# Performance work log

Hardware: AMD Instinct MI355X
Metric: run time of the kernel (lower is better)

Reference implementation:

```python
import jax, jax.numpy as jnp
import numpy as np

B, CIN, COUT, H, W = 16, 128, 128, 64, 64
E, PS, FF = 8, 16, 8
GC, HID, HC = 4 * FF, 64, COUT * 4  # gate_channel, gate hidden, bottleneck hidden


def conv(x, w, stride=1, pad=0, groups=1):
    # x: [B,C,H,W], w: [O,I/groups,kh,kw]
    return jax.lax.conv_general_dilated(
        x, w, (stride, stride), [(pad, pad), (pad, pad)], feature_group_count=groups)


def group_norm(x, scale, bias, groups, eps=1e-5):
    b, c = x.shape[:2]
    xr = x.reshape(b, groups, c // groups, *x.shape[2:])
    m = xr.mean(axis=(2, 3, 4), keepdims=True)
    v = xr.var(axis=(2, 3, 4), keepdims=True)
    xr = (xr - m) * jax.lax.rsqrt(v + eps)
    return xr.reshape(x.shape) * scale[None, :, None, None] + bias[None, :, None, None]


def setup_inputs() -> dict:
    key = jax.random.key(0)
    ks = jax.random.split(key, 8)
    f = lambda k, shp: jax.random.normal(k, shp, jnp.float32) * 0.05
    return dict(
        x=jax.random.normal(ks[0], (B, CIN, H, W), jnp.float32),
        w_exp=f(ks[1], (E, COUT, CIN, 3, 3)),
        gn_exp_s=jnp.ones((E, COUT), jnp.float32),
        gn_exp_b=jnp.zeros((E, COUT), jnp.float32),
        w1=f(ks[2], (GC, HID)), b1=jnp.zeros((HID,), jnp.float32),
        w2=f(ks[3], (HID, E)), b2=jnp.zeros((E,), jnp.float32),
        w_pw1=f(ks[4], (HC, COUT, 1, 1)),
        gn1_s=jnp.ones((HC,), jnp.float32), gn1_b=jnp.zeros((HC,), jnp.float32),
        w_dw=f(ks[5], (HC, 1, 3, 3)),
        gn2_s=jnp.ones((HC,), jnp.float32), gn2_b=jnp.zeros((HC,), jnp.float32),
        w_pw2=f(ks[6], (COUT, HC, 1, 1)),
        gn3_s=jnp.ones((COUT,), jnp.float32), gn3_b=jnp.zeros((COUT,), jnp.float32),
    )


def reference(x, w_exp, gn_exp_s, gn_exp_b, w1, b1, w2, b2,
              w_pw1, gn1_s, gn1_b, w_dw, gn2_s, gn2_b, w_pw2, gn3_s, gn3_b):
    # ---- Conv experts (residual 3x3 conv + GN + SiLU), vmapped over experts ----
    def expert(w, s, b):
        y = conv(x, w, pad=1)
        y = group_norm(y, s, b, groups=min(8, COUT))
        return jax.nn.silu(y) + x  # use_residual=True, CIN == COUT

    ys = jax.vmap(expert)(w_exp, gn_exp_s, gn_exp_b)  # [E,B,C,H,W]

    # ---- Router gate: Fourier features of patch-center coordinates ----
    ph, pw = H // PS, W // PS
    cy = (jnp.arange(ph, dtype=jnp.float32) + 0.5) / ph
    cx = (jnp.arange(pw, dtype=jnp.float32) + 0.5) / pw
    freqs = (2.0 ** jnp.arange(FF, dtype=jnp.float32)) * jnp.pi
    ay = cy[:, None] * freqs  # [ph,FF]
    ax = cx[:, None] * freqs  # [pw,FF]
    feats = jnp.concatenate([
        jnp.broadcast_to(jnp.sin(ay)[:, None, :], (ph, pw, FF)),
        jnp.broadcast_to(jnp.cos(ay)[:, None, :], (ph, pw, FF)),
        jnp.broadcast_to(jnp.sin(ax)[None, :, :], (ph, pw, FF)),
        jnp.broadcast_to(jnp.cos(ax)[None, :, :], (ph, pw, FF)),
    ], axis=-1)  # [ph,pw,4*FF] == gate_channel
    hgate = jax.nn.silu(feats @ w1 + b1)
    wts = jax.nn.softmax(hgate @ w2 + b2, axis=-1)  # [ph,pw,E]

    # ---- Patch-wise combine of expert outputs ----
    wmap = jnp.repeat(jnp.repeat(wts, PS, axis=0), PS, axis=1)  # [H,W,E]
    combined = jnp.einsum('ebchw,hwe->bchw', ys, wmap)

    # ---- Inverted bottleneck: 1x1 -> dw3x3 -> 1x1(stride2) with GN+SiLU ----
    h = jax.nn.silu(group_norm(conv(combined, w_pw1), gn1_s, gn1_b, groups=8))
    h = jax.nn.silu(group_norm(conv(h, w_dw, pad=1, groups=HC), gn2_s, gn2_b, groups=8))
    h = jax.nn.silu(group_norm(conv(h, w_pw2, stride=2), gn3_s, gn3_b, groups=8))
    return h  # [B, COUT, H//2, W//2]
```

## Files before the change

### kernel.cpp

```cpp
#include <hip/hip_runtime.h>
#include <hip/hip_bf16.h>


#define B_ 16
#define CIN_ 128
#define COUT_ 128
#define H_ 64
#define W_ 64
#define HW_ 4096
#define E_ 8
#define FF_ 8
#define GC_ 32
#define HID_ 64
#define HC_ 512

typedef __hip_bfloat16 bf16;
typedef __bf16 bf16x8 __attribute__((ext_vector_type(8)));
typedef float f32x4 __attribute__((ext_vector_type(4)));
typedef float f32x16 __attribute__((ext_vector_type(16)));

__device__ __forceinline__ float siluf(float v) {
  return v * __builtin_amdgcn_rcpf(1.f + __expf(-v));
}
__device__ __forceinline__ float bf2f(bf16 v) { return __bfloat162float(v); }
__device__ __forceinline__ bf16 f2bf(float v) { return __float2bfloat16(v); }

__device__ __forceinline__ void async16(void* lds, const void* g) {
  __builtin_amdgcn_global_load_lds(
      (const __attribute__((address_space(1))) unsigned int*)g,
      (__attribute__((address_space(3))) unsigned int*)lds, 16, 0, 0);
}

__global__ __launch_bounds__(256) void prep_kernel(
    const float* __restrict__ x, bf16* __restrict__ xT,
    const float* __restrict__ w_exp, bf16* __restrict__ wT,
    const float* __restrict__ w_pw1, const float* __restrict__ w_pw2,
    bf16* __restrict__ wp1T, bf16* __restrict__ wp2T,
    const float* __restrict__ w1, const float* __restrict__ b1,
    const float* __restrict__ w2, const float* __restrict__ b2,
    float* __restrict__ wts) {
  __shared__ float t[128][65];
  int blk = blockIdx.x;
  int tid = threadIdx.x;

  if (blk < 1024) {
    int b = blk >> 6, h = blk & 63;
    int w = tid & 63, c4 = tid >> 6;
    const float* xb = x + ((size_t)(b * 128) * 64 + h) * 64;
#pragma unroll 4
    for (int rep = 0; rep < 32; ++rep) {
      int ci = rep * 4 + c4;
      t[ci][w] = xb[(size_t)ci * HW_ + w];
    }
    __syncthreads();
    bf16* dst = xT + (size_t)(b * 64 + h) * 8192;
#pragma unroll 4
    for (int rep = 0; rep < 32; ++rep) {
      int o = rep * 256 + tid;
      int cg = o >> 9, w2 = (o >> 3) & 63, lo = o & 7;
      dst[o] = f2bf(t[cg * 8 + lo][w2]);
    }
  } else if (blk < 5632) {
    int idx = (blk - 1024) * 256 + tid;
    if (idx < 1179648) {
      int lo = idx & 7;
      int co = (idx >> 3) & 127;
      int cg = (idx >> 10) & 15;
      int rest = idx >> 14;
      int tap = rest % 9, e = rest / 9;
      int ci = cg * 8 + lo;
      wT[idx] = f2bf(w_exp[(((size_t)(e * 128 + co) * 128 + ci) * 9) + tap]);
    }
  } else if (blk < 6144) {
    int idx = (blk - 5632) * 256 + tid;
    if (idx < 65536) wp1T[idx] = f2bf(w_pw1[idx]);
    else wp2T[idx - 65536] = f2bf(w_pw2[idx - 65536]);
  } else {
    uint4* z = (uint4*)((char*)wts + 1024);
    for (int i = tid; i < 960; i += 256) z[i] = make_uint4(0u, 0u, 0u, 0u);
    int p = tid;
    if (p >= 16) return;
    int i = p >> 2, j = p & 3;
    float cy = (i + 0.5f) * 0.25f;
    float cx = (j + 0.5f) * 0.25f;
    float feats[GC_];
#pragma unroll
    for (int f = 0; f < FF_; ++f) {
      float fr = 3.14159265358979f * (float)(1 << f);
      float ay = cy * fr, ax = cx * fr;
      feats[f] = sinf(ay);
      feats[FF_ + f] = cosf(ay);
      feats[2 * FF_ + f] = sinf(ax);
      feats[3 * FF_ + f] = cosf(ax);
    }
    float hid[HID_];
    for (int k = 0; k < HID_; ++k) {
      float a = b1[k];
#pragma unroll
      for (int m = 0; m < GC_; ++m) a = fmaf(feats[m], w1[m * HID_ + k], a);
      hid[k] = siluf(a);
    }
    float lg[E_];
    float mx = -1e30f;
#pragma unroll
    for (int e = 0; e < E_; ++e) {
      float a = b2[e];
      for (int k = 0; k < HID_; ++k) a = fmaf(hid[k], w2[k * E_ + e], a);
      lg[e] = a;
      mx = fmaxf(mx, a);
    }
    float s = 0.f;
#pragma unroll
    for (int e = 0; e < E_; ++e) { lg[e] = __expf(lg[e] - mx); s += lg[e]; }
    float inv = 1.f / s;
#pragma unroll
    for (int e = 0; e < E_; ++e) wts[p * E_ + e] = lg[e] * inv;
  }
}

__global__ __launch_bounds__(256, 2) void conv_mfma(
    const bf16* __restrict__ xT, const bf16* __restrict__ wT,
    float* __restrict__ statsE, bf16* __restrict__ ys, int e_base) {
  __shared__ __align__(16) char xls[4 * 6336];
  __shared__ __align__(16) char wls[2][3 * 8192];
  __shared__ float red[4][8][2];

  int blk = blockIdx.x;
  int xcd = blk & 7;
  int r2 = blk >> 3;
  int b = xcd * 2 + (r2 & 1);
  int rest = r2 >> 1;
  int rt = rest & 15, e = e_base + (rest >> 4);

  int tid = threadIdx.x, lane = tid & 63, wave = tid >> 6;
  int hi = lane >> 5, l31 = lane & 31;
  int h0 = rt * 4;

  if (tid < 48) {
    int cg = tid / 12, rem = tid % 12;
    int r = rem >> 1, edge = rem & 1;
    *(uint4*)(xls + cg * 6336 + r * 1056 + edge * 1040) = make_uint4(0u, 0u, 0u, 0u);
  }
  int rbad = (rt == 0) ? 0 : (rt == 15 ? 5 : -1);
  if (rbad >= 0) {
    int cg = tid >> 6, slot = (tid & 63) + 1;
    *(uint4*)(xls + cg * 6336 + rbad * 1056 + slot * 16) = make_uint4(0u, 0u, 0u, 0u);
  }

  f32x16 acc[4][2];
#pragma unroll
  for (int mt = 0; mt < 4; ++mt)
#pragma unroll
    for (int nt = 0; nt < 2; ++nt)
#pragma unroll
      for (int r = 0; r < 16; ++r) acc[mt][nt][r] = 0.f;

  for (int q = 0; q < 4; ++q) {
    if (q) __syncthreads();
    {
      int cg = wave;
#pragma unroll
      for (int r = 0; r < 6; ++r) {
        int h = h0 - 1 + r;
        if ((unsigned)h < 64u) {
          const char* g = (const char*)xT +
              ((size_t)((b * 64 + h) * 16) + q * 4 + cg) * 1024 + lane * 16;
          async16(xls + cg * 6336 + r * 1056 + 16, g);
        }
      }
    }
#pragma unroll
    for (int s = 0; s < 6; ++s) {
      int seg = wave * 6 + s;
      int tap = seg >> 3, rem = seg & 7;
      int cg = rem >> 1, cb = rem & 1;
      const char* g = (const char*)wT +
          ((size_t)(((e * 9 + tap) * 16) + q * 4 + cg) * 128 + cb * 64) * 16 + lane * 16;
      async16(wls[0] + (tap * 4 + cg) * 2048 + cb * 1024, g);
    }
    __syncthreads();

    for (int dr = 0; dr < 3; ++dr) {
      int buf = dr & 1;
      if (dr < 2) {
#pragma unroll
        for (int s = 0; s < 6; ++s) {
          int seg = wave * 6 + s;
          int tap = seg >> 3, rem = seg & 7;
          int cg = rem >> 1, cb = rem & 1;
          const char* g = (const char*)wT +
              ((size_t)(((e * 9 + (dr + 1) * 3 + tap) * 16) + q * 4 + cg) * 128 + cb * 64) * 16 +
              lane * 16;
          async16(wls[buf ^ 1] + (tap * 4 + cg) * 2048 + cb * 1024, g);
        }
      }
      int r_local = wave + dr;
      const char* wb = wls[buf];
      const char* xrow = xls;
      bf16x8 afp[2][2], bfp[2][2];
      {
        int cgl = hi;
        afp[0][0] = *(const bf16x8*)(wb + cgl * 2048 + (0 * 32 + l31) * 16);
        afp[0][1] = *(const bf16x8*)(wb + cgl * 2048 + (1 * 32 + l31) * 16);
        const char* xr = xrow + cgl * 6336 + r_local * 1056;
        bfp[0][0] = *(const bf16x8*)(xr + (0 * 32 + l31 + 0) * 16);
        bfp[0][1] = *(const bf16x8*)(xr + (1 * 32 + l31 + 0) * 16);
      }
#pragma unroll
      for (int s = 0; s < 12; ++s) {
        int mh = s & 1;
        int cura = s & 1, curb = (s >> 1) & 1;
        if (s < 11) {
          int s1 = s + 1;
          int ds1 = s1 >> 2, ks1 = (s1 >> 1) & 1, mh1 = s1 & 1;
          int cgl1 = ks1 * 2 + hi;
          const char* wt1 = wb + ds1 * 8192 + cgl1 * 2048;
          afp[s1 & 1][0] = *(const bf16x8*)(wt1 + ((mh1 * 2 + 0) * 32 + l31) * 16);
          afp[s1 & 1][1] = *(const bf16x8*)(wt1 + ((mh1 * 2 + 1) * 32 + l31) * 16);
          if (mh1 == 0) {
            const char* xr1 = xrow + cgl1 * 6336 + r_local * 1056;
            bfp[(s1 >> 1) & 1][0] = *(const bf16x8*)(xr1 + (0 * 32 + l31 + ds1) * 16);
            bfp[(s1 >> 1) & 1][1] = *(const bf16x8*)(xr1 + (1 * 32 + l31 + ds1) * 16);
          }
        }
#pragma unroll
        for (int i = 0; i < 2; ++i)
#pragma unroll
          for (int nt = 0; nt < 2; ++nt)
            acc[mh * 2 + i][nt] = __builtin_amdgcn_mfma_f32_32x32x16_bf16(
                afp[cura][i], bfp[curb][nt], acc[mh * 2 + i][nt], 0, 0, 0);
      }
      if (dr < 2) __syncthreads();
    }
  }

  int hh = h0 + wave;
  bf16* yb = ys + (size_t)((e * 16 + b) * 128) * 4096;
#pragma unroll
  for (int mt = 0; mt < 4; ++mt) {
    float s0 = 0.f, ss0 = 0.f, s1 = 0.f, ss1 = 0.f;
#pragma unroll
    for (int nt = 0; nt < 2; ++nt) {
      int w = nt * 32 + l31;
      int pos = hh * 64 + w;
#pragma unroll
      for (int r = 0; r < 16; ++r) {
        float v = acc[mt][nt][r];
        if (r < 8) { s0 += v; ss0 += v * v; } else { s1 += v; ss1 += v * v; }
        int row = (r & 3) + 8 * (r >> 2) + 4 * hi;
        yb[(size_t)(mt * 32 + row) * 4096 + pos] = f2bf(v);
      }
    }
#pragma unroll
    for (int off = 32; off; off >>= 1) {
      s0 += __shfl_down(s0, off, 64);
      ss0 += __shfl_down(ss0, off, 64);
      s1 += __shfl_down(s1, off, 64);
      ss1 += __shfl_down(ss1, off, 64);
    }
    if (lane == 0) {
      red[wave][mt * 2][0] = s0; red[wave][mt * 2][1] = ss0;
      red[wave][mt * 2 + 1][0] = s1; red[wave][mt * 2 + 1][1] = ss1;
    }
  }
  __syncthreads();
  if (tid < 16) {
    int g = tid >> 1, which = tid & 1;
    float t = red[0][g][which] + red[1][g][which] + red[2][g][which] + red[3][g][which];
    atomicAdd(&statsE[((e * 16 + b) * 8 + g) * 2 + which], t);
  }
}

__global__ __launch_bounds__(256) void combine_cl(
    const float* __restrict__ x, const bf16* __restrict__ ys,
    const float* __restrict__ stE, const float* __restrict__ gns,
    const float* __restrict__ gnb, const float* __restrict__ wts,
    bf16* __restrict__ ccl) {
  __shared__ bf16 tile[64][132];
  int blk = blockIdx.x;
  int xcd = blk & 7;
  int k2 = blk >> 3;
  int b = xcd * 2 + (k2 >> 6);
  int h = k2 & 63;
  int t = threadIdx.x;
  int oct = t & 7, cq = t >> 3;
  int w0 = oct * 8;
  int gidx = cq >> 2;
  int pid = (h >> 4) * 4 + (w0 >> 4);
  int pos = h * 64 + w0;

  float m_[8], r_[8], wt_[8];
#pragma unroll
  for (int e = 0; e < 8; ++e) {
    float S = stE[((e * 16 + b) * 8 + gidx) * 2];
    float SS = stE[((e * 16 + b) * 8 + gidx) * 2 + 1];
    float mean = S * (1.f / 65536.f);
    float var = SS * (1.f / 65536.f) - mean * mean;
    m_[e] = mean;
    r_[e] = rsqrtf(var + 1e-5f);
    wt_[e] = wts[pid * 8 + e];
  }

#pragma unroll
  for (int k = 0; k < 4; ++k) {
    int co = cq * 4 + k;
    const float* xp = x + ((size_t)(b * 128 + co) << 12) + pos;
    float v[8];
    float4 xa = *(const float4*)xp;
    float4 xb2 = *(const float4*)(xp + 4);
    v[0] = xa.x; v[1] = xa.y; v[2] = xa.z; v[3] = xa.w;
    v[4] = xb2.x; v[5] = xb2.y; v[6] = xb2.z; v[7] = xb2.w;
#pragma unroll
    for (int e = 0; e < 8; ++e) {
      uint4 u = *(const uint4*)(ys + ((size_t)((e * 16 + b) * 128 + co) << 12) + pos);
      const bf16* pv = (const bf16*)&u;
      float sc = r_[e] * gns[e * 128 + co];
      float sh = gnb[e * 128 + co] - m_[e] * sc;
#pragma unroll
      for (int j = 0; j < 8; ++j) {
        float yn = bf2f(pv[j]) * sc + sh;
        v[j] = fmaf(siluf(yn), wt_[e], v[j]);
      }
    }
#pragma unroll
    for (int j = 0; j < 8; ++j) tile[w0 + j][co] = f2bf(v[j]);
  }
  __syncthreads();
  int row = t >> 2, q = t & 3;
  char* dst = (char*)ccl + ((size_t)(b * 4096 + h * 64 + row)) * 256 + q * 64;
  const char* src = (const char*)&tile[row][0] + q * 64;
#pragma unroll
  for (int i = 0; i < 4; ++i)
    *(uint4*)(dst + i * 16) = *(const uint4*)(src + i * 16);
}

__global__ __launch_bounds__(256) void pw1_mfma(
    const bf16* __restrict__ ccl, const bf16* __restrict__ wp1T,
    bf16* __restrict__ h1cl, float* __restrict__ stats1) {
  __shared__ __align__(16) char bls[32768];
  __shared__ __align__(16) char ls2[34816];
  __shared__ float red[4][2][2];
  int blk = blockIdx.x;
  int n0 = blk * 128;
  int t = threadIdx.x, lane = t & 63, wave = t >> 6;
  int quad = lane >> 4, l15 = lane & 15;
  int b = n0 >> 12;

#pragma unroll
  for (int i = 0; i < 8; ++i) {
    int id = t + 256 * i;
    int r = id >> 4, c = id & 15;
    *(uint4*)(bls + c * 2048 + r * 16) =
        *(const uint4*)((const char*)ccl + (size_t)(n0 + r) * 256 + c * 16);
  }

  for (int mtile = 0; mtile < 4; ++mtile) {
    int m0 = mtile * 128;
    char* als = ls2;
#pragma unroll
    for (int i = 0; i < 8; ++i) {
      int id = t + 256 * i;
      int r = id >> 4, c = id & 15;
      *(uint4*)(als + c * 2048 + r * 16) =
          *(const uint4*)((const char*)wp1T + (size_t)(m0 + r) * 256 + c * 16);
    }
    __syncthreads();

    f32x4 acc[8][2];
#pragma unroll
    for (int mt = 0; mt < 8; ++mt)
#pragma unroll
      for (int nt = 0; nt < 2; ++nt) acc[mt][nt] = (f32x4){0.f, 0.f, 0.f, 0.f};

#pragma unroll
    for (int kc = 0; kc < 4; ++kc) {
      int cgq = kc * 4 + quad;
      bf16x8 af[8];
#pragma unroll
      for (int mt = 0; mt < 8; ++mt)
        af[mt] = *(const bf16x8*)(als + cgq * 2048 + (mt * 16 + l15) * 16);
      bf16x8 bfr[2];
#pragma unroll
      for (int nt = 0; nt < 2; ++nt)
        bfr[nt] = *(const bf16x8*)(bls + cgq * 2048 + (wave * 32 + nt * 16 + l15) * 16);
#pragma unroll
      for (int mt = 0; mt < 8; ++mt)
#pragma unroll
        for (int nt = 0; nt < 2; ++nt)
          acc[mt][nt] = __builtin_amdgcn_mfma_f32_16x16x32_bf16(
              af[mt], bfr[nt], acc[mt][nt], 0, 0, 0);
    }

    __syncthreads();
    float s[2] = {0.f, 0.f}, ss[2] = {0.f, 0.f};
    bf16* tile = (bf16*)ls2;
#pragma unroll
    for (int mt = 0; mt < 8; ++mt) {
      int gi = mt >> 2;
#pragma unroll
      for (int nt = 0; nt < 2; ++nt) {
        int n = wave * 32 + nt * 16 + l15;
#pragma unroll
        for (int r = 0; r < 4; ++r) {
          float v = acc[mt][nt][r];
          s[gi] += v;
          ss[gi] += v * v;
          tile[n * 132 + mt * 16 + quad * 4 + r] = f2bf(v);
        }
      }
    }
#pragma unroll
    for (int gi = 0; gi < 2; ++gi) {
#pragma unroll
      for (int off = 32; off; off >>= 1) {
        s[gi] += __shfl_down(s[gi], off, 64);
        ss[gi] += __shfl_down(ss[gi], off, 64);
      }
    }
    if (lane == 0) {
      red[wave][0][0] = s[0]; red[wave][0][1] = ss[0];
      red[wave][1][0] = s[1]; red[wave][1][1] = ss[1];
    }
    __syncthreads();
    if (t < 4) {
      int gi = t >> 1, which = t & 1;
      float v = red[0][gi][which] + red[1][gi][which] + red[2][gi][which] + red[3][gi][which];
      atomicAdd(&stats1[(b * 8 + mtile * 2 + gi) * 2 + which], v);
    }
#pragma unroll
    for (int i = 0; i < 8; ++i) {
      int id = t + 256 * i;
      int r = id >> 4, q = id & 15;
      char* dst = (char*)h1cl + (size_t)(n0 + r) * 1024 + m0 * 2 + q * 16;
      const char* src = (const char*)tile + r * 264 + q * 16;
      *(uint4*)dst = *(const uint4*)src;
    }
    __syncthreads();
  }
}

__global__ __launch_bounds__(256) void dw_cl(
    const bf16* __restrict__ h1cl, const float* __restrict__ w_dw,
    const float* __restrict__ st1, const float* __restrict__ gs,
    const float* __restrict__ gb, bf16* __restrict__ h2cl,
    float* __restrict__ stats2) {
  __shared__ __align__(16) bf16 tile[18 * 66 * 16];
  __shared__ float red2[4][2];
  int blk = blockIdx.x;
  int ht = blk & 3, hcg = (blk >> 2) & 31, b = blk >> 7;
  int h0 = ht * 16;
  int hc0 = hcg * 16;
  int hcb = hcg >> 2;
  int t = threadIdx.x;

  float S1 = st1[(b * 8 + hcb) * 2], SS1 = st1[(b * 8 + hcb) * 2 + 1];
  float mean = S1 * (1.f / 262144.f);
  float var1 = SS1 * (1.f / 262144.f) - mean * mean;
  float rstd = rsqrtf(var1 + 1e-5f);
  float scale[16], shift[16];
#pragma unroll
  for (int j = 0; j < 16; ++j) {
    float g = gs[hc0 + j];
    scale[j] = rstd * g;
    shift[j] = gb[hc0 + j] - mean * rstd * g;
  }

  for (int i = 0; i < 5; ++i) {
    int idx = t + 256 * i;
    if (idx >= 1188) break;
    int row = idx / 66, wslot = idx - row * 66;
    int hh = h0 - 1 + row;
    int w = wslot - 1;
    int swz = (wslot >> 2) & 3;
    bf16* dst = tile + (row * 66 + wslot) * 16;
    if ((unsigned)hh < 64u && (unsigned)w < 64u) {
      const char* p = (const char*)h1cl + ((size_t)(b * 4096 + hh * 64 + w) * 512 + hc0) * 2;
      uint4 a0 = *(const uint4*)p;
      uint4 a1 = *(const uint4*)(p + 16);
      const bf16* pv = (const bf16*)&a0;
      const bf16* pv1 = (const bf16*)&a1;
      bf16 outv[16];
#pragma unroll
      for (int j = 0; j < 8; ++j)
        outv[j] = f2bf(siluf(bf2f(pv[j]) * scale[j] + shift[j]));
#pragma unroll
      for (int j = 0; j < 8; ++j)
        outv[8 + j] = f2bf(siluf(bf2f(pv1[j]) * scale[8 + j] + shift[8 + j]));
#pragma unroll
      for (int qq = 0; qq < 4; ++qq) {
        int ph = (qq + swz) & 3;
        *(uint2*)(dst + ph * 4) = *(const uint2*)(outv + qq * 4);
      }
    } else {
      *(uint4*)dst = make_uint4(0u, 0u, 0u, 0u);
      *(uint4*)(dst + 8) = make_uint4(0u, 0u, 0u, 0u);
    }
  }
  __syncthreads();

  int w = t & 63, q = t >> 6;
  float wv[9][4];
#pragma unroll
  for (int j = 0; j < 4; ++j) {
    int hc = hc0 + q * 4 + j;
#pragma unroll
    for (int tap = 0; tap < 9; ++tap) wv[tap][j] = w_dw[hc * 9 + tap];
  }

  f32x4 win[3][3];
  float acc_s = 0.f, acc_ss = 0.f;

  auto ld4 = [&](int r, int dwi) -> f32x4 {
    int slot = w + dwi;
    int ph = (q + (slot >> 2)) & 3;
    const bf16* p = tile + (r * 66 + slot) * 16 + ph * 4;
    uint2 u = *(const uint2*)p;
    const bf16* pb = (const bf16*)&u;
    return (f32x4){bf2f(pb[0]), bf2f(pb[1]), bf2f(pb[2]), bf2f(pb[3])};
  };

#pragma unroll
  for (int dwi = 0; dwi < 3; ++dwi) {
    win[0][dwi] = ld4(0, dwi);
    win[1][dwi] = ld4(1, dwi);
  }
#pragma unroll
  for (int orow = 0; orow < 16; ++orow) {
    int rnew = orow + 2;
    int ringn = rnew % 3;
#pragma unroll
    for (int dwi = 0; dwi < 3; ++dwi) win[ringn][dwi] = ld4(rnew, dwi);
    f32x4 acc = (f32x4){0.f, 0.f, 0.f, 0.f};
#pragma unroll
    for (int dr = 0; dr < 3; ++dr) {
      int ring = (orow + dr) % 3;
#pragma unroll
      for (int dwi = 0; dwi < 3; ++dwi) {
#pragma unroll
        for (int j = 0; j < 4; ++j)
          acc[j] = fmaf(win[ring][dwi][j], wv[dr * 3 + dwi][j], acc[j]);
      }
    }
#pragma unroll
    for (int j = 0; j < 4; ++j) { acc_s += acc[j]; acc_ss += acc[j] * acc[j]; }
    if (!(orow & 1) && !(w & 1)) {
      int hglob = h0 + orow;
      int pos2 = (hglob >> 1) * 32 + (w >> 1);
      bf16 tmp[4];
#pragma unroll
      for (int j = 0; j < 4; ++j) tmp[j] = f2bf(acc[j]);
      *(uint2*)((char*)h2cl + ((size_t)(b * 1024 + pos2) * 512 + hc0 + q * 4) * 2) =
          *(const uint2*)tmp;
    }
  }

#pragma unroll
  for (int off = 32; off; off >>= 1) {
    acc_s += __shfl_down(acc_s, off, 64);
    acc_ss += __shfl_down(acc_ss, off, 64);
  }
  int wave = t >> 6;
  if ((t & 63) == 0) { red2[wave][0] = acc_s; red2[wave][1] = acc_ss; }
  __syncthreads();
  if (t < 2) {
    float v = red2[0][t] + red2[1][t] + red2[2][t] + red2[3][t];
    atomicAdd(&stats2[(b * 8 + hcb) * 2 + t], v);
  }
}

__global__ __launch_bounds__(256) void pw2_mfma(
    const bf16* __restrict__ h2, const bf16* __restrict__ wp2T,
    const float* __restrict__ st2, const float* __restrict__ gs2,
    const float* __restrict__ gb2, float* __restrict__ h3,
    float* __restrict__ stats3) {
  __shared__ __align__(16) char als[2][4096];
  __shared__ __align__(16) char bls[2][4096];
  __shared__ float red[4][4][2];
  int blk = blockIdx.x;
  int mhalf = blk >> 8;
  int nblk = blk & 255;
  int n0 = nblk * 64;
  int m0 = mhalf * 64;
  int b = n0 >> 10, posb = n0 & 1023;
  int t = threadIdx.x, lane = t & 63, wave = t >> 6;
  int quad = lane >> 4, l15 = lane & 15;
  int wbase = wave * 16;
  int c4 = t >> 6, r = t & 63;

  auto load_bls = [&](char* dst, int kc) {
    int hc0 = (kc * 4 + c4) * 8;
    int g = hc0 >> 6;
    float S = st2[(b * 8 + g) * 2], SS = st2[(b * 8 + g) * 2 + 1];
    float mean = S * (1.f / 262144.f);
    float rstd = rsqrtf(SS * (1.f / 262144.f) - mean * mean + 1e-5f);
    uint4 u = *(const uint4*)((const char*)h2 + (size_t)(n0 + r) * 1024 +
                              (size_t)(kc * 4 + c4) * 16);
    const bf16* pv = (const bf16*)&u;
    bf16 outv[8];
#pragma unroll
    for (int j = 0; j < 8; ++j) {
      float xv = bf2f(pv[j]);
      xv = (xv - mean) * rstd * gs2[hc0 + j] + gb2[hc0 + j];
      outv[j] = f2bf(siluf(xv));
    }
    *(uint4*)dst = *(const uint4*)outv;
  };
  auto load_als = [&](char* dstbase, int kc) {
    *(uint4*)(dstbase + c4 * 1024 + r * 16) =
        *(const uint4*)((const char*)wp2T + (size_t)(m0 + r) * 1024 +
                        (size_t)(kc * 4 + c4) * 16);
  };

  f32x4 acc[4];
#pragma unroll
  for (int mt = 0; mt < 4; ++mt) acc[mt] = (f32x4){0.f, 0.f, 0.f, 0.f};

  {
    load_als(als[0], 0);
    load_bls(bls[0] + c4 * 1024 + r * 16, 0);
  }
#pragma unroll
  for (int kc = 0; kc < 16; ++kc) {
    __syncthreads();
    if (kc + 1 < 16) {
      int nb = (kc + 1) & 1;
      load_als(als[nb], kc + 1);
      load_bls(bls[nb] + c4 * 1024 + r * 16, kc + 1);
    }
    int buf = kc & 1;
    bf16x8 bf1 = *(const bf16x8*)(bls[buf] + quad * 1024 + (wbase + l15) * 16);
#pragma unroll
    for (int mt = 0; mt < 4; ++mt) {
      bf16x8 af = *(const bf16x8*)(als[buf] + quad * 1024 + (mt * 16 + l15) * 16);
      acc[mt] = __builtin_amdgcn_mfma_f32_16x16x32_bf16(af, bf1, acc[mt], 0, 0, 0);
    }
  }

#pragma unroll
  for (int mt = 0; mt < 4; ++mt) {
    float s = 0.f, ss = 0.f;
    int pos = posb + wbase + l15;
#pragma unroll
    for (int rr = 0; rr < 4; ++rr) {
      float v = acc[mt][rr];
      s += v;
      ss += v * v;
      int co = m0 + mt * 16 + quad * 4 + rr;
      h3[(size_t)(b * 128 + co) * 1024 + pos] = v;
    }
#pragma unroll
    for (int off = 32; off; off >>= 1) {
      s += __shfl_down(s, off, 64);
      ss += __shfl_down(ss, off, 64);
    }
    if (lane == 0) { red[wave][mt][0] = s; red[wave][mt][1] = ss; }
  }
  __syncthreads();
  if (t < 8) {
    int mt = t >> 1, which = t & 1;
    float v = red[0][mt][which] + red[1][mt][which] + red[2][mt][which] + red[3][mt][which];
    atomicAdd(&stats3[(b * 8 + mhalf * 4 + mt) * 2 + which], v);
  }
}

__global__ void out_kernel(const float* __restrict__ h3, const float* __restrict__ stats,
                           const float* __restrict__ gs, const float* __restrict__ gb,
                           float* __restrict__ out) {
  const int total4 = (B_ * COUT_ * 1024) >> 2;
  for (int i4 = blockIdx.x * blockDim.x + threadIdx.x; i4 < total4;
       i4 += gridDim.x * blockDim.x) {
    int idx = i4 << 2;
    int c = (idx >> 10) & 127;
    int b = idx >> 17;
    int bg = b * 8 + (c >> 4);
    float S = stats[bg * 2], SS = stats[bg * 2 + 1];
    float mean = S * (1.f / 16384.f);
    float var = SS * (1.f / 16384.f) - mean * mean;
    float rstd = rsqrtf(var + 1e-5f);
    float sc = rstd * gs[c];
    float sh = gb[c] - mean * sc;
    float4 hv = *(const float4*)(h3 + idx);
    float4 res;
    res.x = siluf(hv.x * sc + sh);
    res.y = siluf(hv.y * sc + sh);
    res.z = siluf(hv.z * sc + sh);
    res.w = siluf(hv.w * sc + sh);
    *(float4*)(out + idx) = res;
  }
}

extern "C" void kernel_launch(void* const* d_in, const int* in_sizes, int n_in,
                              void* d_out, int out_size, void* d_ws, size_t ws_size,
                              hipStream_t stream) {
  const float* x = (const float*)d_in[0];
  const float* w_exp = (const float*)d_in[1];
  const float* gn_exp_s = (const float*)d_in[2];
  const float* gn_exp_b = (const float*)d_in[3];
  const float* w1 = (const float*)d_in[4];
  const float* b1 = (const float*)d_in[5];
  const float* w2 = (const float*)d_in[6];
  const float* b2 = (const float*)d_in[7];
  const float* w_pw1 = (const float*)d_in[8];
  const float* gn1_s = (const float*)d_in[9];
  const float* gn1_b = (const float*)d_in[10];
  const float* w_dw = (const float*)d_in[11];
  const float* gn2_s = (const float*)d_in[12];
  const float* gn2_b = (const float*)d_in[13];
  const float* w_pw2 = (const float*)d_in[14];
  const float* gn3_s = (const float*)d_in[15];
  const float* gn3_b = (const float*)d_in[16];

  char* ws = (char*)d_ws;
  const size_t WP1T_OFF = 16384;
  const size_t WP2T_OFF = WP1T_OFF + 131072;
  const size_t XT_OFF = WP2T_OFF + 131072;
  const size_t WT_OFF = XT_OFF + 16777216;
  const size_t YS_OFF = WT_OFF + 2359296;
  const size_t NEEDED = YS_OFF + 134217728;
  if (ws_size < NEEDED) return;

  float* wts = (float*)ws;
  float* stats1 = (float*)(ws + 1024);
  float* stats2 = (float*)(ws + 2048);
  float* stats3 = (float*)(ws + 3072);
  float* statsE = (float*)(ws + 4096);
  bf16* wp1T = (bf16*)(ws + WP1T_OFF);
  bf16* wp2T = (bf16*)(ws + WP2T_OFF);
  bf16* xT = (bf16*)(ws + XT_OFF);
  bf16* ccl = (bf16*)(ws + XT_OFF);
  bf16* wT = (bf16*)(ws + WT_OFF);
  bf16* ys = (bf16*)(ws + YS_OFF);
  bf16* h1cl = (bf16*)(ws + YS_OFF);
  bf16* h2cl = (bf16*)(ws + YS_OFF + 67108864);
  float* h3 = (float*)(ws + YS_OFF + 83886080);

  prep_kernel<<<6145, 256, 0, stream>>>(x, xT, w_exp, wT, w_pw1, w_pw2, wp1T, wp2T,
                                        w1, b1, w2, b2, wts);
  conv_mfma<<<1024, 256, 0, stream>>>(xT, wT, statsE, ys, 0);
  conv_mfma<<<1024, 256, 0, stream>>>(xT, wT, statsE, ys, 4);
  combine_cl<<<B_ * 64, 256, 0, stream>>>(x, ys, statsE, gn_exp_s, gn_exp_b, wts, ccl);
  pw1_mfma<<<512, 256, 0, stream>>>(ccl, wp1T, h1cl, stats1);
  dw_cl<<<B_ * 32 * 4, 256, 0, stream>>>(h1cl, w_dw, stats1, gn1_s, gn1_b, h2cl, stats2);
  pw2_mfma<<<512, 256, 0, stream>>>(h2cl, wp2T, stats2, gn2_s, gn2_b, h3, stats3);
  out_kernel<<<1024, 256, 0, stream>>>(h3, stats3, gn3_s, gn3_b, (float*)d_out);
}
```

Baseline: 432.9 us.

## Fuse expert combine into pw1 GEMM and merge expert conv launches

Adds a combine_pw1 kernel that builds the GN+SiLU+gated expert combination for two image rows directly in shared memory and immediately runs the 1x1 pw1 MFMA GEMM on it. This avoids writing the combined tensor to global memory and reading it back. The two conv_mfma launches are also merged into one 2048-block grid. The fused path needs a larger workspace so h1 does not overwrite ys, and it falls back to the old path if the workspace is too small.

Measured after the change: 451.3 us. +4.3%, slower.

```diff
diff --git a/kernel.cpp b/kernel.cpp
--- a/kernel.cpp
+++ b/kernel.cpp
@@ -120,7 +120,7 @@
 
 __global__ __launch_bounds__(256, 2) void conv_mfma(
     const bf16* __restrict__ xT, const bf16* __restrict__ wT,
-    float* __restrict__ statsE, bf16* __restrict__ ys, int e_base) {
+    float* __restrict__ statsE, bf16* __restrict__ ys) {
   __shared__ __align__(16) char xls[4 * 6336];
   __shared__ __align__(16) char wls[2][3 * 8192];
   __shared__ float red[4][8][2];
@@ -130,7 +130,7 @@
   int r2 = blk >> 3;
   int b = xcd * 2 + (r2 & 1);
   int rest = r2 >> 1;
-  int rt = rest & 15, e = e_base + (rest >> 4);
+  int rt = rest & 15, e = rest >> 4;
 
   int tid = threadIdx.x, lane = tid & 63, wave = tid >> 6;
   int hi = lane >> 5, l31 = lane & 31;
@@ -268,6 +268,161 @@
     int g = tid >> 1, which = tid & 1;
     float t = red[0][g][which] + red[1][g][which] + red[2][g][which] + red[3][g][which];
     atomicAdd(&statsE[((e * 16 + b) * 8 + g) * 2 + which], t);
+  }
+}
+
+__global__ __launch_bounds__(256) void combine_pw1(
+    const float* __restrict__ x, const bf16* __restrict__ ys,
+    const float* __restrict__ stE, const float* __restrict__ gns,
+    const float* __restrict__ gnb, const float* __restrict__ wts,
+    const bf16* __restrict__ wp1T, bf16* __restrict__ h1cl,
+    float* __restrict__ stats1) {
+  __shared__ __align__(16) char bls[32768];
+  __shared__ __align__(16) char ls2[34816];
+  __shared__ float red[4][2][2];
+
+  int blk = blockIdx.x;
+  int xcd = blk & 7;
+  int rest = blk >> 3;
+  int b = xcd * 2 + (rest & 1);
+  int hpair = rest >> 1;
+  int h0 = hpair * 2;
+  int n0 = b * 4096 + h0 * 64;
+
+  int t = threadIdx.x, lane = t & 63, wave = t >> 6;
+  int quad = lane >> 4, l15 = lane & 15;
+
+  {
+    int oct = t & 7, cq = t >> 3;
+    int w0 = oct * 8;
+    int gidx = cq >> 2;
+    int pid = (h0 >> 4) * 4 + (w0 >> 4);
+
+    float m_[8], r_[8], wt_[8];
+#pragma unroll
+    for (int e = 0; e < 8; ++e) {
+      float S = stE[((e * 16 + b) * 8 + gidx) * 2];
+      float SS = stE[((e * 16 + b) * 8 + gidx) * 2 + 1];
+      float mean = S * (1.f / 65536.f);
+      float var = SS * (1.f / 65536.f) - mean * mean;
+      m_[e] = mean;
+      r_[e] = rsqrtf(var + 1e-5f);
+      wt_[e] = wts[pid * 8 + e];
+    }
+
+#pragma unroll
+    for (int hh = 0; hh < 2; ++hh) {
+      int pos = (h0 + hh) * 64 + w0;
+#pragma unroll
+      for (int k = 0; k < 4; ++k) {
+        int co = cq * 4 + k;
+        const float* xp = x + ((size_t)(b * 128 + co) << 12) + pos;
+        float v[8];
+        float4 xa = *(const float4*)xp;
+        float4 xb2 = *(const float4*)(xp + 4);
+        v[0] = xa.x; v[1] = xa.y; v[2] = xa.z; v[3] = xa.w;
+        v[4] = xb2.x; v[5] = xb2.y; v[6] = xb2.z; v[7] = xb2.w;
+#pragma unroll
+        for (int e = 0; e < 8; ++e) {
+          uint4 u = *(const uint4*)(ys + ((size_t)((e * 16 + b) * 128 + co) << 12) + pos);
+          const bf16* pv = (const bf16*)&u;
+          float sc = r_[e] * gns[e * 128 + co];
+          float sh = gnb[e * 128 + co] - m_[e] * sc;
+#pragma unroll
+          for (int j = 0; j < 8; ++j) {
+            float yn = bf2f(pv[j]) * sc + sh;
+            v[j] = fmaf(siluf(yn), wt_[e], v[j]);
+          }
+        }
+        bf16* bb = (bf16*)bls + (co >> 3) * 1024 + (hh * 64 + w0) * 8 + (co & 7);
+#pragma unroll
+        for (int j = 0; j < 8; ++j) bb[j * 8] = f2bf(v[j]);
+      }
+    }
+  }
+
+  for (int mtile = 0; mtile < 4; ++mtile) {
+    int m0 = mtile * 128;
+    char* als = ls2;
+#pragma unroll
+    for (int i = 0; i < 8; ++i) {
+      int id = t + 256 * i;
+      int r = id >> 4, c = id & 15;
+      *(uint4*)(als + c * 2048 + r * 16) =
+          *(const uint4*)((const char*)wp1T + (size_t)(m0 + r) * 256 + c * 16);
+    }
+    __syncthreads();
+
+    f32x4 acc[8][2];
+#pragma unroll
+    for (int mt = 0; mt < 8; ++mt)
+#pragma unroll
+      for (int nt = 0; nt < 2; ++nt) acc[mt][nt] = (f32x4){0.f, 0.f, 0.f, 0.f};
+
+#pragma unroll
+    for (int kc = 0; kc < 4; ++kc) {
+      int cgq = kc * 4 + quad;
+      bf16x8 af[8];
+#pragma unroll
+      for (int mt = 0; mt < 8; ++mt)
+        af[mt] = *(const bf16x8*)(als + cgq * 2048 + (mt * 16 + l15) * 16);
+      bf16x8 bfr[2];
+#pragma unroll
+      for (int nt = 0; nt < 2; ++nt)
+        bfr[nt] = *(const bf16x8*)(bls + cgq * 2048 + (wave * 32 + nt * 16 + l15) * 16);
+#pragma unroll
+      for (int mt = 0; mt < 8; ++mt)
+#pragma unroll
+        for (int nt = 0; nt < 2; ++nt)
+          acc[mt][nt] = __builtin_amdgcn_mfma_f32_16x16x32_bf16(
+              af[mt], bfr[nt], acc[mt][nt], 0, 0, 0);
+    }
+
+    __syncthreads();
+    float s[2] = {0.f, 0.f}, ss[2] = {0.f, 0.f};
+    bf16* tile = (bf16*)ls2;
+#pragma unroll
+    for (int mt = 0; mt < 8; ++mt) {
+      int gi = mt >> 2;
+#pragma unroll
+      for (int nt = 0; nt < 2; ++nt) {
+        int n = wave * 32 + nt * 16 + l15;
+#pragma unroll
+        for (int r = 0; r < 4; ++r) {
+          float v = acc[mt][nt][r];
+          s[gi] += v;
+          ss[gi] += v * v;
+          tile[n * 132 + mt * 16 + quad * 4 + r] = f2bf(v);
+        }
+      }
+    }
+#pragma unroll
+    for (int gi = 0; gi < 2; ++gi) {
+#pragma unroll
+      for (int off = 32; off; off >>= 1) {
+        s[gi] += __shfl_down(s[gi], off, 64);
+        ss[gi] += __shfl_down(ss[gi], off, 64);
+      }
+    }
+    if (lane == 0) {
+      red[wave][0][0] = s[0]; red[wave][0][1] = ss[0];
+      red[wave][1][0] = s[1]; red[wave][1][1] = ss[1];
+    }
+    __syncthreads();
+    if (t < 4) {
+      int gi = t >> 1, which = t & 1;
+      float v = red[0][gi][which] + red[1][gi][which] + red[2][gi][which] + red[3][gi][which];
+      atomicAdd(&stats1[(b * 8 + mtile * 2 + gi) * 2 + which], v);
+    }
+#pragma unroll
+    for (int i = 0; i < 8; ++i) {
+      int id = t + 256 * i;
+      int r = id >> 4, q = id & 15;
+      char* dst = (char*)h1cl + (size_t)(n0 + r) * 1024 + m0 * 2 + q * 16;
+      const char* src = (const char*)tile + r * 264 + q * 16;
+      *(uint4*)dst = *(const uint4*)src;
+    }
+    __syncthreads();
   }
 }
 
@@ -717,7 +872,10 @@
   const size_t WT_OFF = XT_OFF + 16777216;
   const size_t YS_OFF = WT_OFF + 2359296;
   const size_t NEEDED = YS_OFF + 134217728;
+  const size_t H1_OFF = YS_OFF + 134217728;
+  const size_t NEEDED_BIG = H1_OFF + 67108864;
   if (ws_size < NEEDED) return;
+  bool big = ws_size >= NEEDED_BIG;
 
   float* wts = (float*)ws;
   float* stats1 = (float*)(ws + 1024);
@@ -727,20 +885,31 @@
   bf16* wp1T = (bf16*)(ws + WP1T_OFF);
   bf16* wp2T = (bf16*)(ws + WP2T_OFF);
   bf16* xT = (bf16*)(ws + XT_OFF);
-  bf16* ccl = (bf16*)(ws + XT_OFF);
   bf16* wT = (bf16*)(ws + WT_OFF);
   bf16* ys = (bf16*)(ws + YS_OFF);
-  bf16* h1cl = (bf16*)(ws + YS_OFF);
-  bf16* h2cl = (bf16*)(ws + YS_OFF + 67108864);
-  float* h3 = (float*)(ws + YS_OFF + 83886080);
 
   prep_kernel<<<6145, 256, 0, stream>>>(x, xT, w_exp, wT, w_pw1, w_pw2, wp1T, wp2T,
                                         w1, b1, w2, b2, wts);
-  conv_mfma<<<1024, 256, 0, stream>>>(xT, wT, statsE, ys, 0);
-  conv_mfma<<<1024, 256, 0, stream>>>(xT, wT, statsE, ys, 4);
-  combine_cl<<<B_ * 64, 256, 0, stream>>>(x, ys, statsE, gn_exp_s, gn_exp_b, wts, ccl);
-  pw1_mfma<<<512, 256, 0, stream>>>(ccl, wp1T, h1cl, stats1);
-  dw_cl<<<B_ * 32 * 4, 256, 0, stream>>>(h1cl, w_dw, stats1, gn1_s, gn1_b, h2cl, stats2);
-  pw2_mfma<<<512, 256, 0, stream>>>(h2cl, wp2T, stats2, gn2_s, gn2_b, h3, stats3);
-  out_kernel<<<1024, 256, 0, stream>>>(h3, stats3, gn3_s, gn3_b, (float*)d_out);
-}
+  conv_mfma<<<2048, 256, 0, stream>>>(xT, wT, statsE, ys);
+
+  if (big) {
+    bf16* h1cl = (bf16*)(ws + H1_OFF);
+    bf16* h2cl = (bf16*)(ws + YS_OFF);
+    float* h3 = (float*)(ws + YS_OFF + 16777216);
+    combine_pw1<<<512, 256, 0, stream>>>(x, ys, statsE, gn_exp_s, gn_exp_b, wts,
+                                         wp1T, h1cl, stats1);
+    dw_cl<<<B_ * 32 * 4, 256, 0, stream>>>(h1cl, w_dw, stats1, gn1_s, gn1_b, h2cl, stats2);
+    pw2_mfma<<<512, 256, 0, stream>>>(h2cl, wp2T, stats2, gn2_s, gn2_b, h3, stats3);
+    out_kernel<<<1024, 256, 0, stream>>>(h3, stats3, gn3_s, gn3_b, (float*)d_out);
+  } else {
+    bf16* ccl = (bf16*)(ws + XT_OFF);
+    bf16* h1cl = (bf16*)(ws + YS_OFF);
+    bf16* h2cl = (bf16*)(ws + YS_OFF + 67108864);
+    float* h3 = (float*)(ws + YS_OFF + 83886080);
+    combine_cl<<<B_ * 64, 256, 0, stream>>>(x, ys, statsE, gn_exp_s, gn_exp_b, wts, ccl);
+    pw1_mfma<<<512, 256, 0, stream>>>(ccl, wp1T, h1cl, stats1);
+    dw_cl<<<B_ * 32 * 4, 256, 0, stream>>>(h1cl, w_dw, stats1, gn1_s, gn1_b, h2cl, stats2);
+    pw2_mfma<<<512, 256, 0, stream>>>(h2cl, wp2T, stats2, gn2_s, gn2_b, h3, stats3);
+    out_kernel<<<1024, 256, 0, stream>>>(h3, stats3, gn3_s, gn3_b, (float*)d_out);
+  }
+}
```
